# Kernel tuning notes

Measured on AMD Instinct MI355X. Metric: run time of the kernel, lower is better.

Reference implementation:

```python
import jax, jax.numpy as jnp
import numpy as np

B, S, D, H = 4, 2048, 1024, 16

def setup_inputs() -> dict:
    key = jax.random.key(0)
    ks = jax.random.split(key, 8)
    s = D ** -0.5
    return {
        "query": jax.random.normal(ks[0], (B, S, D), jnp.float32),
        "bias": jnp.zeros((B, 1, 1, S), jnp.float32),
        "Wq": jax.random.normal(ks[1], (D, D), jnp.float32) * s,
        "bq": jnp.zeros((D,), jnp.float32),
        "Wk": jax.random.normal(ks[2], (D, D), jnp.float32) * s,
        "bk": jnp.zeros((D,), jnp.float32),
        "Wv": jax.random.normal(ks[3], (D, D), jnp.float32) * s,
        "bv": jnp.zeros((D,), jnp.float32),
        "Wo": jax.random.normal(ks[4], (D, D), jnp.float32) * s,
        "bo": jnp.zeros((D,), jnp.float32),
        "leaky_k": jax.random.normal(ks[5], (1, 1, D), jnp.float32) * s,
        "leaky_v": jax.random.normal(ks[6], (1, 1, D), jnp.float32) * s,
    }

def _split_heads(x, heads):
    b, l, c = x.shape
    return x.reshape(b, l, heads, c // heads).transpose(0, 2, 1, 3)  # [b,h,l,dh]

def reference(query, bias, Wq, bq, Wk, bk, Wv, bv, Wo, bo, leaky_k, leaky_v):
    q = query @ Wq.T + bq
    k = query @ Wk.T + bk
    v = query @ Wv.T + bv
    b = query.shape[0]
    # prepend leaky sink key/value token
    k = jnp.concatenate([jnp.broadcast_to(leaky_k, (b, 1, D)), k], axis=1)
    v = jnp.concatenate([jnp.broadcast_to(leaky_v, (b, 1, D)), v], axis=1)
    qh = _split_heads(q, H) * (D // H) ** -0.5
    kh = _split_heads(k, H)
    vh = _split_heads(v, H)
    logits = jnp.einsum('bhqd,bhkd->bhqk', qh, kh)
    # pad bias with zero column for the sink token
    bias_l = jnp.concatenate([jnp.zeros(bias.shape[:3] + (1,), bias.dtype), bias], axis=-1)
    logits = logits + bias_l
    weights = jax.nn.softmax(logits, axis=-1)
    x = jnp.einsum('bhqk,bhkd->bhqd', weights, vh)
    out = x.transpose(0, 2, 1, 3).reshape(b, -1, D)
    return out @ Wo.T + bo
```

## Files before the change

kernel.cpp:

```cpp
#include <hip/hip_runtime.h>
#include <cstdint>
#include <cstddef>

#define DEV static __device__ __forceinline__

typedef __attribute__((ext_vector_type(8))) __bf16 bf16x8;
typedef __attribute__((ext_vector_type(8))) unsigned short u16x8;
typedef __attribute__((ext_vector_type(4))) float f32x4;

#define BB 4
#define SS 2048
#define DD 1024
#define HH 16
#define DH 64
#define SK 2049

DEV unsigned short f2bf(float f) {
  unsigned int u = __builtin_bit_cast(unsigned int, f);
  u += 0x7fffu + ((u >> 16) & 1u);
  return (unsigned short)(u >> 16);
}
DEV float bf2f(unsigned short h) {
  unsigned int u = ((unsigned int)h) << 16;
  return __builtin_bit_cast(float, u);
}

DEV void gl_lds16(const void* g, void* l) {
  __builtin_amdgcn_global_load_lds(
      (const __attribute__((address_space(1))) void*)g,
      (__attribute__((address_space(3))) void*)l, 16, 0, 0);
}

DEV f32x4 mfma_bf16(bf16x8 a, bf16x8 b, f32x4 c) {
  return __builtin_amdgcn_mfma_f32_16x16x32_bf16(a, b, c, 0, 0, 0);
}

__global__ __launch_bounds__(256) void k_convert_query(const float* __restrict__ src,
                                                       unsigned short* __restrict__ dst) {
  int i = blockIdx.x * 256 + threadIdx.x;
  float4 v = reinterpret_cast<const float4*>(src)[i];
  ushort4 o;
  o.x = f2bf(v.x); o.y = f2bf(v.y); o.z = f2bf(v.z); o.w = f2bf(v.w);
  reinterpret_cast<ushort4*>(dst)[i] = o;
}

__global__ __launch_bounds__(256) void k_convert_w(const float* __restrict__ w0,
                                                   const float* __restrict__ w1,
                                                   const float* __restrict__ w2,
                                                   const float* __restrict__ w3,
                                                   unsigned short* __restrict__ wqkv,
                                                   unsigned short* __restrict__ wo) {
  int i = blockIdx.x * 256 + threadIdx.x;
  int e = i * 4;
  int sec = e >> 20;
  int off = e & 1048575;
  const float* s = (sec == 0) ? w0 : (sec == 1) ? w1 : (sec == 2) ? w2 : w3;
  float4 v = *reinterpret_cast<const float4*>(s + off);
  ushort4 o;
  o.x = f2bf(v.x); o.y = f2bf(v.y); o.z = f2bf(v.z); o.w = f2bf(v.w);
  unsigned short* d = (sec < 3) ? (wqkv + (size_t)sec * 1048576 + off) : (wo + off);
  *reinterpret_cast<ushort4*>(d) = o;
}

__global__ __launch_bounds__(256) void k_sink(const float* __restrict__ lk,
                                              const float* __restrict__ lv,
                                              unsigned short* __restrict__ Kh,
                                              unsigned short* __restrict__ Vh) {
  int t = blockIdx.x * 256 + threadIdx.x;
  int bh = t >> 6, d = t & 63;
  int h = bh & (HH - 1);
  Kh[(size_t)bh * SK * DH + d] = f2bf(lk[h * DH + d]);
  Vh[(size_t)bh * SK * DH + d] = f2bf(lv[h * DH + d]);
}


__global__ __launch_bounds__(256) void k_gemm_qkv(const unsigned short* __restrict__ A,
                                                  const unsigned short* __restrict__ Bw,
                                                  const float* __restrict__ bq,
                                                  const float* __restrict__ bk,
                                                  const float* __restrict__ bv,
                                                  unsigned short* __restrict__ Qh,
                                                  unsigned short* __restrict__ Kh,
                                                  unsigned short* __restrict__ Vh) {
  __shared__ unsigned short As[128 * 32];
  __shared__ unsigned short Bs[128 * 32];
  const int tid = threadIdx.x, lane = tid & 63, wid = tid >> 6;
  const int g = lane >> 4, l15 = lane & 15;
  const int m0 = blockIdx.x * 128, n0 = blockIdx.y * 128;
  const int wr = (wid >> 1) * 64, wc = (wid & 1) * 64;

  f32x4 acc[4][4] = {};

  for (int k0 = 0; k0 < 1024; k0 += 32) {
    __syncthreads();
#pragma unroll
    for (int i = 0; i < 2; ++i) {
      int e = i * 2048 + wid * 512 + lane * 8;
      int r = e >> 5, c = e & 31;
      gl_lds16(A + (size_t)(m0 + r) * 1024 + k0 + c, &As[i * 2048 + wid * 512]);
      gl_lds16(Bw + (size_t)(n0 + r) * 1024 + k0 + c, &Bs[i * 2048 + wid * 512]);
    }
    __syncthreads();
    bf16x8 af[4], bf[4];
#pragma unroll
    for (int m = 0; m < 4; ++m)
      af[m] = *reinterpret_cast<const bf16x8*>(&As[(wr + m * 16 + l15) * 32 + g * 8]);
#pragma unroll
    for (int n = 0; n < 4; ++n)
      bf[n] = *reinterpret_cast<const bf16x8*>(&Bs[(wc + n * 16 + l15) * 32 + g * 8]);
#pragma unroll
    for (int m = 0; m < 4; ++m)
#pragma unroll
      for (int n = 0; n < 4; ++n)
        acc[m][n] = mfma_bf16(af[m], bf[n], acc[m][n]);
  }

#pragma unroll
  for (int n = 0; n < 4; ++n) {
    int gn = n0 + wc + n * 16 + l15;
    int sec = gn >> 10;
    int nh = gn & 1023;
    int h = nh >> 6, d = nh & 63;
    const float* bias = (sec == 0) ? bq : (sec == 1) ? bk : bv;
    float bia = bias[nh];
#pragma unroll
    for (int m = 0; m < 4; ++m) {
#pragma unroll
      for (int j = 0; j < 4; ++j) {
        int row = m0 + wr + m * 16 + g * 4 + j;
        int b = row >> 11, s = row & 2047;
        float v = acc[m][n][j] + bia;
        if (sec == 0) {
          Qh[((size_t)(b * HH + h) * SS + s) * DH + d] = f2bf(v * 0.125f);
        } else if (sec == 1) {
          Kh[((size_t)(b * HH + h) * SK + s + 1) * DH + d] = f2bf(v);
        } else {
          Vh[((size_t)(b * HH + h) * SK + s + 1) * DH + d] = f2bf(v);
        }
      }
    }
  }
}

__global__ __launch_bounds__(256) void k_gemm_out(const unsigned short* __restrict__ A,
                                                  const unsigned short* __restrict__ Bw,
                                                  const float* __restrict__ bo,
                                                  float* __restrict__ out) {
  __shared__ unsigned short As[128 * 32];
  __shared__ unsigned short Bs[128 * 32];
  const int tid = threadIdx.x, lane = tid & 63, wid = tid >> 6;
  const int g = lane >> 4, l15 = lane & 15;
  const int m0 = blockIdx.x * 128, n0 = blockIdx.y * 128;
  const int wr = (wid >> 1) * 64, wc = (wid & 1) * 64;

  f32x4 acc[4][4] = {};

  for (int k0 = 0; k0 < 1024; k0 += 32) {
    __syncthreads();
#pragma unroll
    for (int i = 0; i < 2; ++i) {
      int e = i * 2048 + wid * 512 + lane * 8;
      int r = e >> 5, c = e & 31;
      gl_lds16(A + (size_t)(m0 + r) * 1024 + k0 + c, &As[i * 2048 + wid * 512]);
      gl_lds16(Bw + (size_t)(n0 + r) * 1024 + k0 + c, &Bs[i * 2048 + wid * 512]);
    }
    __syncthreads();
    bf16x8 af[4], bf[4];
#pragma unroll
    for (int m = 0; m < 4; ++m)
      af[m] = *reinterpret_cast<const bf16x8*>(&As[(wr + m * 16 + l15) * 32 + g * 8]);
#pragma unroll
    for (int n = 0; n < 4; ++n)
      bf[n] = *reinterpret_cast<const bf16x8*>(&Bs[(wc + n * 16 + l15) * 32 + g * 8]);
#pragma unroll
    for (int m = 0; m < 4; ++m)
#pragma unroll
      for (int n = 0; n < 4; ++n)
        acc[m][n] = mfma_bf16(af[m], bf[n], acc[m][n]);
  }

#pragma unroll
  for (int n = 0; n < 4; ++n) {
    int gn = n0 + wc + n * 16 + l15;
    float bia = bo[gn];
#pragma unroll
    for (int m = 0; m < 4; ++m) {
#pragma unroll
      for (int j = 0; j < 4; ++j) {
        int row = m0 + wr + m * 16 + g * 4 + j;
        out[(size_t)row * 1024 + gn] = acc[m][n][j] + bia;
      }
    }
  }
}

__global__ __launch_bounds__(256) void k_attn(const unsigned short* __restrict__ Qh,
                                              const unsigned short* __restrict__ Kh,
                                              const unsigned short* __restrict__ Vh,
                                              const float* __restrict__ bias,
                                              unsigned short* __restrict__ Xbf) {
  __shared__ unsigned short K_lds[2][64 * 64];
  __shared__ unsigned short VT[2][64 * 64];
  __shared__ unsigned short P_lds[4][16 * 64];

  const int tid = threadIdx.x, lane = tid & 63, w = tid >> 6;
  const int g = lane >> 4, c = lane & 15;
  const int idx = blockIdx.x;
  const int bh = idx >> 5, qt = idx & 31;
  const int b = bh >> 4, h = bh & 15;
  const int q0 = qt * 64 + w * 16;
  const size_t qbase = ((size_t)bh * SS + q0) * DH;
  const size_t kvbase = (size_t)bh * SK * DH;

  bf16x8 qf[2];
#pragma unroll
  for (int t = 0; t < 2; ++t)
    qf[t] = *reinterpret_cast<const bf16x8*>(Qh + qbase + (size_t)c * DH + t * 32 + g * 8);

  f32x4 s0 = {0.f, 0.f, 0.f, 0.f};
#pragma unroll
  for (int t = 0; t < 2; ++t) {
    bf16x8 kb = *reinterpret_cast<const bf16x8*>(Kh + kvbase + t * 32 + g * 8);
    s0 = mfma_bf16(qf[t], kb, s0);
  }
  float l_sink[4], lpart[4];
  f32x4 o[4];
#pragma unroll
  for (int j = 0; j < 4; ++j) { l_sink[j] = __expf(s0[j]); lpart[j] = 0.f; }
#pragma unroll
  for (int n = 0; n < 4; ++n) {
    float v = bf2f(Vh[kvbase + n * 16 + c]);
#pragma unroll
    for (int j = 0; j < 4; ++j) o[n][j] = l_sink[j] * v;
  }

  const int kp = tid >> 3;
  const int d0 = (tid & 7) * 8;
  u16x8 pv0, pv1;

  auto stage_k = [&](int key0, unsigned short* Kdst) {
#pragma unroll
    for (int i = 0; i < 2; ++i) {
      int ob = i * 4096 + w * 1024 + lane * 16;
      int r = ob >> 7, cb = ob & 127;
      int sc = cb ^ ((r & 7) << 4);
      gl_lds16(Kh + kvbase + (size_t)(key0 + r + 1) * DH + (sc >> 1),
               (char*)Kdst + i * 4096 + w * 1024);
    }
  };
  auto load_v = [&](int key0) {
    pv0 = *reinterpret_cast<const u16x8*>(Vh + kvbase + (size_t)(key0 + kp * 2 + 1) * DH + d0);
    pv1 = *reinterpret_cast<const u16x8*>(Vh + kvbase + (size_t)(key0 + kp * 2 + 2) * DH + d0);
  };
  auto write_v = [&](unsigned short* VTdst) {
#pragma unroll
    for (int j = 0; j < 8; ++j) {
      int d = d0 + j;
      unsigned int pk = (unsigned int)pv0[j] | ((unsigned int)pv1[j] << 16);
      int byte = (d * 128 + kp * 4) ^ ((j ^ ((d >> 3) & 7)) << 4);
      *(unsigned int*)((char*)VTdst + byte) = pk;
    }
  };

  auto compute_tile = [&](int key0, const unsigned short* Kc, const unsigned short* Vc) {
    f32x4 s[4];
    __builtin_amdgcn_s_setprio(1);
#pragma unroll
    for (int n = 0; n < 4; ++n) {
      f32x4 z = {0.f, 0.f, 0.f, 0.f};
      s[n] = z;
#pragma unroll
      for (int t = 0; t < 2; ++t) {
        int row = n * 16 + c;
        int byte = (row * 128 + t * 64 + g * 16) ^ ((row & 7) << 4);
        bf16x8 kb = *reinterpret_cast<const bf16x8*>((const char*)Kc + byte);
        s[n] = mfma_bf16(qf[t], kb, s[n]);
      }
    }
    __builtin_amdgcn_s_setprio(0);

    unsigned short* Pw = P_lds[w];
#pragma unroll
    for (int n = 0; n < 4; ++n) {
      float bia = bias[(size_t)b * SS + key0 + n * 16 + c];
#pragma unroll
      for (int j = 0; j < 4; ++j) {
        float p = __expf(s[n][j] + bia);
        lpart[j] += p;
        int row = g * 4 + j;
        int byte = (row * 128 + (n * 16 + c) * 2) ^ ((row & 7) << 4);
        *(unsigned short*)((char*)Pw + byte) = f2bf(p);
      }
    }
    bf16x8 pa[2];
#pragma unroll
    for (int t = 0; t < 2; ++t) {
      int byte = (c * 128 + t * 64 + g * 16) ^ ((c & 7) << 4);
      pa[t] = *reinterpret_cast<const bf16x8*>((char*)Pw + byte);
    }
    __builtin_amdgcn_s_setprio(1);
#pragma unroll
    for (int n = 0; n < 4; ++n) {
#pragma unroll
      for (int t = 0; t < 2; ++t) {
        int rv = n * 16 + c;
        int byte = (rv * 128 + t * 64 + g * 16) ^ (((rv & 7) ^ ((rv >> 3) & 7)) << 4);
        bf16x8 vb = *reinterpret_cast<const bf16x8*>((const char*)Vc + byte);
        o[n] = mfma_bf16(pa[t], vb, o[n]);
      }
    }
    __builtin_amdgcn_s_setprio(0);
  };

  stage_k(0, K_lds[0]);
  load_v(0);
  write_v(VT[0]);
  __syncthreads();

  for (int kt = 0; kt < 32; kt += 2) {
    stage_k((kt + 1) * 64, K_lds[1]);
    load_v((kt + 1) * 64);
    compute_tile(kt * 64, K_lds[0], VT[0]);
    write_v(VT[1]);
    __syncthreads();

    if (kt + 2 < 32) {
      stage_k((kt + 2) * 64, K_lds[0]);
      load_v((kt + 2) * 64);
    }
    compute_tile((kt + 1) * 64, K_lds[1], VT[1]);
    if (kt + 2 < 32) write_v(VT[0]);
    __syncthreads();
  }

#pragma unroll
  for (int mask = 1; mask < 16; mask <<= 1)
#pragma unroll
    for (int j = 0; j < 4; ++j)
      lpart[j] += __shfl_xor(lpart[j], mask, 64);

#pragma unroll
  for (int j = 0; j < 4; ++j) {
    float inv = 1.f / (l_sink[j] + lpart[j]);
    int q = q0 + g * 4 + j;
    size_t base = ((size_t)b * SS + q) * DD + h * DH + c;
#pragma unroll
    for (int n = 0; n < 4; ++n)
      Xbf[base + n * 16] = f2bf(o[n][j] * inv);
  }
}

extern "C" void kernel_launch(void* const* d_in, const int* in_sizes, int n_in,
                              void* d_out, int out_size, void* d_ws, size_t ws_size,
                              hipStream_t stream) {
  const float* query = (const float*)d_in[0];
  const float* bias  = (const float*)d_in[1];
  const float* Wq = (const float*)d_in[2];
  const float* bq = (const float*)d_in[3];
  const float* Wk = (const float*)d_in[4];
  const float* bk = (const float*)d_in[5];
  const float* Wv = (const float*)d_in[6];
  const float* bv = (const float*)d_in[7];
  const float* Wo = (const float*)d_in[8];
  const float* bo = (const float*)d_in[9];
  const float* lk = (const float*)d_in[10];
  const float* lv = (const float*)d_in[11];

  char* ws = (char*)d_ws;
  unsigned short* Wqkv = (unsigned short*)(ws);
  unsigned short* Wob  = (unsigned short*)(ws + 6291456);
  unsigned short* Qbf  = (unsigned short*)(ws + 8388608);
  unsigned short* Qh   = (unsigned short*)(ws + 25165824);
  unsigned short* Kh   = (unsigned short*)(ws + 41943040);
  unsigned short* Vh   = (unsigned short*)(ws + 58728448);
  unsigned short* Xbf  = Qbf;
  float* out = (float*)d_out;

  k_convert_query<<<8192, 256, 0, stream>>>(query, Qbf);
  k_convert_w<<<4096, 256, 0, stream>>>(Wq, Wk, Wv, Wo, Wqkv, Wob);
  k_sink<<<16, 256, 0, stream>>>(lk, lv, Kh, Vh);
  dim3 g1(64, 24);
  k_gemm_qkv<<<g1, 256, 0, stream>>>(Qbf, Wqkv, bq, bk, bv, Qh, Kh, Vh);
  k_attn<<<2048, 256, 0, stream>>>(Qh, Kh, Vh, bias, Xbf);
  dim3 g2(64, 8);
  k_gemm_out<<<g2, 256, 0, stream>>>(Xbf, Wob, bo, out);
}
```

Baseline: 360.6 us.

## Process two query fragments per wave in attention and use exp2 softmax

Each attention wave now handles 32 query rows (two 16-row fragments) instead of 16, so every K/V tile staged into LDS is reused by twice as many MFMAs and the grid halves to 1024 blocks. The log2(e) factor is folded into the Q scaling and into the bias, so the softmax can use the native exp2 instruction instead of expf. Float-to-bf16 conversion switches to the compiler's __bf16 cast instead of the hand-written rounding. In exchange, accumulator and register use per wave roughly doubles, which may reduce occupancy, and the block count may underfill the GPU.

```diff
diff --git a/kernel.cpp b/kernel.cpp
--- a/kernel.cpp
+++ b/kernel.cpp
@@ -14,6 +14,7 @@
 #define HH 16
 #define DH 64
 #define SK 2049
+#define LOG2E 1.4426950408889634f
 
 DEV unsigned short f2bf(float f) {
   unsigned int u = __builtin_bit_cast(unsigned int, f);
@@ -131,7 +132,7 @@
         int b = row >> 11, s = row & 2047;
         float v = acc[m][n][j] + bia;
         if (sec == 0) {
-          Qh[((size_t)(b * HH + h) * SS + s) * DH + d] = f2bf(v * 0.125f);
+          Qh[((size_t)(b * HH + h) * SS + s) * DH + d] = f2bf(v * (0.125f * LOG2E));
         } else if (sec == 1) {
           Kh[((size_t)(b * HH + h) * SK + s + 1) * DH + d] = f2bf(v);
         } else {
@@ -206,32 +207,44 @@
   const int tid = threadIdx.x, lane = tid & 63, w = tid >> 6;
   const int g = lane >> 4, c = lane & 15;
   const int idx = blockIdx.x;
-  const int bh = idx >> 5, qt = idx & 31;
+  const int bh = idx >> 4, qt = idx & 15;
   const int b = bh >> 4, h = bh & 15;
-  const int q0 = qt * 64 + w * 16;
-  const size_t qbase = ((size_t)bh * SS + q0) * DH;
+  const int q0 = qt * 128 + w * 32;
   const size_t kvbase = (size_t)bh * SK * DH;
-
-  bf16x8 qf[2];
+  const size_t bbase = (size_t)b * SS;
+
+  bf16x8 qf[2][2];
+#pragma unroll
+  for (int f = 0; f < 2; ++f)
+#pragma unroll
+    for (int t = 0; t < 2; ++t)
+      qf[f][t] = *reinterpret_cast<const bf16x8*>(
+          Qh + ((size_t)bh * SS + q0 + f * 16) * DH + (size_t)c * DH + t * 32 + g * 8);
+
+  bf16x8 kb_sink[2];
 #pragma unroll
   for (int t = 0; t < 2; ++t)
-    qf[t] = *reinterpret_cast<const bf16x8*>(Qh + qbase + (size_t)c * DH + t * 32 + g * 8);
-
-  f32x4 s0 = {0.f, 0.f, 0.f, 0.f};
-#pragma unroll
-  for (int t = 0; t < 2; ++t) {
-    bf16x8 kb = *reinterpret_cast<const bf16x8*>(Kh + kvbase + t * 32 + g * 8);
-    s0 = mfma_bf16(qf[t], kb, s0);
-  }
-  float l_sink[4], lpart[4];
-  f32x4 o[4];
-#pragma unroll
-  for (int j = 0; j < 4; ++j) { l_sink[j] = __expf(s0[j]); lpart[j] = 0.f; }
+    kb_sink[t] = *reinterpret_cast<const bf16x8*>(Kh + kvbase + t * 32 + g * 8);
+  float l_sink[2][4], lpart[2][4];
+  f32x4 o[2][4];
+#pragma unroll
+  for (int f = 0; f < 2; ++f) {
+    f32x4 s0 = {0.f, 0.f, 0.f, 0.f};
+#pragma unroll
+    for (int t = 0; t < 2; ++t) s0 = mfma_bf16(qf[f][t], kb_sink[t], s0);
+#pragma unroll
+    for (int j = 0; j < 4; ++j) {
+      l_sink[f][j] = __builtin_amdgcn_exp2f(s0[j]);
+      lpart[f][j] = 0.f;
+    }
+  }
 #pragma unroll
   for (int n = 0; n < 4; ++n) {
     float v = bf2f(Vh[kvbase + n * 16 + c]);
 #pragma unroll
-    for (int j = 0; j < 4; ++j) o[n][j] = l_sink[j] * v;
+    for (int f = 0; f < 2; ++f)
+#pragma unroll
+      for (int j = 0; j < 4; ++j) o[f][n][j] = l_sink[f][j] * v;
   }
 
   const int kp = tid >> 3;
@@ -263,41 +276,49 @@
   };
 
   auto compute_tile = [&](int key0, const unsigned short* Kc, const unsigned short* Vc) {
-    f32x4 s[4];
+    float bia[4];
+#pragma unroll
+    for (int n = 0; n < 4; ++n)
+      bia[n] = bias[bbase + key0 + n * 16 + c] * LOG2E;
+
+    f32x4 s[2][4];
     __builtin_amdgcn_s_setprio(1);
 #pragma unroll
     for (int n = 0; n < 4; ++n) {
       f32x4 z = {0.f, 0.f, 0.f, 0.f};
-      s[n] = z;
+      s[0][n] = z; s[1][n] = z;
 #pragma unroll
       for (int t = 0; t < 2; ++t) {
         int row = n * 16 + c;
         int byte = (row * 128 + t * 64 + g * 16) ^ ((row & 7) << 4);
         bf16x8 kb = *reinterpret_cast<const bf16x8*>((const char*)Kc + byte);
-        s[n] = mfma_bf16(qf[t], kb, s[n]);
+        s[0][n] = mfma_bf16(qf[0][t], kb, s[0][n]);
+        s[1][n] = mfma_bf16(qf[1][t], kb, s[1][n]);
       }
     }
     __builtin_amdgcn_s_setprio(0);
 
     unsigned short* Pw = P_lds[w];
-#pragma unroll
-    for (int n = 0; n < 4; ++n) {
-      float bia = bias[(size_t)b * SS + key0 + n * 16 + c];
-#pragma unroll
-      for (int j = 0; j < 4; ++j) {
-        float p = __expf(s[n][j] + bia);
-        lpart[j] += p;
-        int row = g * 4 + j;
-        int byte = (row * 128 + (n * 16 + c) * 2) ^ ((row & 7) << 4);
-        *(unsigned short*)((char*)Pw + byte) = f2bf(p);
-      }
-    }
-    bf16x8 pa[2];
-#pragma unroll
-    for (int t = 0; t < 2; ++t) {
-      int byte = (c * 128 + t * 64 + g * 16) ^ ((c & 7) << 4);
-      pa[t] = *reinterpret_cast<const bf16x8*>((char*)Pw + byte);
-    }
+    bf16x8 pa[2][2];
+#pragma unroll
+    for (int f = 0; f < 2; ++f) {
+#pragma unroll
+      for (int n = 0; n < 4; ++n)
+#pragma unroll
+        for (int j = 0; j < 4; ++j) {
+          float p = __builtin_amdgcn_exp2f(s[f][n][j] + bia[n]);
+          lpart[f][j] += p;
+          int row = g * 4 + j;
+          int byte = (row * 128 + (n * 16 + c) * 2) ^ ((row & 7) << 4);
+          *(__bf16*)((char*)Pw + byte) = (__bf16)p;
+        }
+#pragma unroll
+      for (int t = 0; t < 2; ++t) {
+        int byte = (c * 128 + t * 64 + g * 16) ^ ((c & 7) << 4);
+        pa[f][t] = *reinterpret_cast<const bf16x8*>((char*)Pw + byte);
+      }
+    }
+
     __builtin_amdgcn_s_setprio(1);
 #pragma unroll
     for (int n = 0; n < 4; ++n) {
@@ -306,7 +327,8 @@
         int rv = n * 16 + c;
         int byte = (rv * 128 + t * 64 + g * 16) ^ (((rv & 7) ^ ((rv >> 3) & 7)) << 4);
         bf16x8 vb = *reinterpret_cast<const bf16x8*>((const char*)Vc + byte);
-        o[n] = mfma_bf16(pa[t], vb, o[n]);
+        o[0][n] = mfma_bf16(pa[0][t], vb, o[0][n]);
+        o[1][n] = mfma_bf16(pa[1][t], vb, o[1][n]);
       }
     }
     __builtin_amdgcn_s_setprio(0);
@@ -336,18 +358,24 @@
 #pragma unroll
   for (int mask = 1; mask < 16; mask <<= 1)
 #pragma unroll
-    for (int j = 0; j < 4; ++j)
-      lpart[j] += __shfl_xor(lpart[j], mask, 64);
-
-#pragma unroll
-  for (int j = 0; j < 4; ++j) {
-    float inv = 1.f / (l_sink[j] + lpart[j]);
-    int q = q0 + g * 4 + j;
-    size_t base = ((size_t)b * SS + q) * DD + h * DH + c;
-#pragma unroll
-    for (int n = 0; n < 4; ++n)
-      Xbf[base + n * 16] = f2bf(o[n][j] * inv);
-  }
+    for (int f = 0; f < 2; ++f)
+#pragma unroll
+      for (int j = 0; j < 4; ++j)
+        lpart[f][j] += __shfl_xor(lpart[f][j], mask, 64);
+
+#pragma unroll
+  for (int f = 0; f < 2; ++f)
+#pragma unroll
+    for (int j = 0; j < 4; ++j) {
+      float inv = 1.f / (l_sink[f][j] + lpart[f][j]);
+      int q = q0 + f * 16 + g * 4 + j;
+      size_t base = (bbase + q) * DD + h * DH + c;
+#pragma unroll
+      for (int n = 0; n < 4; ++n) {
+        __bf16 hv = (__bf16)(o[f][n][j] * inv);
+        Xbf[base + n * 16] = __builtin_bit_cast(unsigned short, hv);
+      }
+    }
 }
 
 extern "C" void kernel_launch(void* const* d_in, const int* in_sizes, int n_in,
@@ -381,7 +409,7 @@
   k_sink<<<16, 256, 0, stream>>>(lk, lv, Kh, Vh);
   dim3 g1(64, 24);
   k_gemm_qkv<<<g1, 256, 0, stream>>>(Qbf, Wqkv, bq, bk, bv, Qh, Kh, Vh);
-  k_attn<<<2048, 256, 0, stream>>>(Qh, Kh, Vh, bias, Xbf);
+  k_attn<<<1024, 256, 0, stream>>>(Qh, Kh, Vh, bias, Xbf);
   dim3 g2(64, 8);
   k_gemm_out<<<g2, 256, 0, stream>>>(Xbf, Wob, bo, out);
 }
```

Measured after the change: 337.2 us. -6.5%, faster.
